# Performance work log

Measured on AMD Instinct MI355X. Metric: run time of the kernel, lower is better.

The kernel has to match this reference:

```python
import jax, jax.numpy as jnp
import numpy as np

B, L, C = 2, 2048, 1024
H = 16
D = C // H  # 64
MAX_SCALE_MUL = float(np.log(100.0))
EPS = 1e-12


def setup_inputs() -> dict:
    key = jax.random.key(0)
    ks = jax.random.split(key, 6)
    x = jax.random.normal(ks[0], (B, L, C), dtype=jnp.float32)
    attn_bias = jax.random.normal(ks[1], (1, 1, L, L), dtype=jnp.float32) * 0.02
    W_qkv = jax.random.normal(ks[2], (3 * C, C), dtype=jnp.float32) * (1.0 / np.sqrt(C))
    q_bias = jnp.zeros((C,), dtype=jnp.float32)
    v_bias = jnp.zeros((C,), dtype=jnp.float32)
    scale_mul = jnp.full((1, H, 1, 1), np.log(4.0), dtype=jnp.float32)
    W_proj = jax.random.normal(ks[3], (C, C), dtype=jnp.float32) * (1.0 / np.sqrt(C))
    b_proj = jnp.zeros((C,), dtype=jnp.float32)
    return {"x": x, "attn_bias": attn_bias, "W_qkv": W_qkv, "q_bias": q_bias,
            "v_bias": v_bias, "scale_mul": scale_mul, "W_proj": W_proj, "b_proj": b_proj}


def _l2norm(t):
    # F.normalize(dim=-1): x / max(||x||_2, eps)
    n = jnp.sqrt(jnp.sum(t * t, axis=-1, keepdims=True))
    return t / jnp.maximum(n, EPS)


def reference(x, attn_bias, W_qkv, q_bias, v_bias, scale_mul, W_proj, b_proj):
    bias = jnp.concatenate([q_bias, jnp.zeros_like(q_bias), v_bias])  # (3C,)
    qkv = x @ W_qkv.T + bias                     # (B, L, 3C)
    qkv = qkv.reshape(B, L, 3, H, D)
    q, k, v = jnp.moveaxis(qkv, 2, 0)            # each (B, L, H, D)
    q = jnp.transpose(q, (0, 2, 1, 3))           # (B, H, L, D)
    k = jnp.transpose(k, (0, 2, 1, 3))
    v = jnp.transpose(v, (0, 2, 1, 3))
    # attn_l2_norm path: scale = 1, learned per-head scale clamped at log(100)
    sm = jnp.exp(jnp.minimum(scale_mul, MAX_SCALE_MUL))  # (1, H, 1, 1)
    q = _l2norm(q) * sm
    k = _l2norm(k)
    scores = jnp.einsum('bhqd,bhkd->bhqk', q, k) + attn_bias  # scale=1
    attn = jax.nn.softmax(scores, axis=-1)
    out = jnp.einsum('bhqk,bhkd->bhqd', attn, v)  # (B, H, L, D)
    out = jnp.transpose(out, (0, 2, 1, 3)).reshape(B, L, C)
    return out @ W_proj.T + b_proj
```

## Files before the change

kernel.cpp:

```cpp
#include <hip/hip_runtime.h>


typedef __bf16 bf16x8 __attribute__((ext_vector_type(8)));
typedef __bf16 bf16x4 __attribute__((ext_vector_type(4)));
typedef float  f32x4  __attribute__((ext_vector_type(4)));

#define BB 2
#define LL 2048
#define CC 1024
#define HH 16
#define DD 64
#define LOG2E 1.44269504088896f

__device__ __forceinline__ f32x4 mfma_16x16x32(bf16x8 a, bf16x8 b, f32x4 c) {
    return __builtin_amdgcn_mfma_f32_16x16x32_bf16(a, b, c, 0, 0, 0);
}

__device__ __forceinline__ void gload_lds16(const __bf16* g, __bf16* lds) {
    __builtin_amdgcn_global_load_lds(
        (const __attribute__((address_space(1))) unsigned int*)g,
        (__attribute__((address_space(3))) unsigned int*)lds,
        16, 0, 0);
}

__device__ __forceinline__ unsigned pk_bf16(float a, float b) {
    unsigned short ua = __builtin_bit_cast(unsigned short, (__bf16)a);
    unsigned short ub = __builtin_bit_cast(unsigned short, (__bf16)b);
    return (unsigned)ua | ((unsigned)ub << 16);
}

__global__ __launch_bounds__(256) void cvt3_kernel(
    const float* __restrict__ x, const float* __restrict__ wq, const float* __restrict__ wp,
    __bf16* __restrict__ xb, __bf16* __restrict__ wqb, __bf16* __restrict__ wpb) {
    const int i = blockIdx.x * 256 + threadIdx.x;
    const float* src; __bf16* dst; int off;
    if (i < 1048576)      { src = x;  dst = xb;  off = i; }
    else if (i < 1835008) { src = wq; dst = wqb; off = i - 1048576; }
    else                  { src = wp; dst = wpb; off = i - 1835008; }
    float4 v = reinterpret_cast<const float4*>(src)[off];
    bf16x4 o;
    o[0] = (__bf16)v.x; o[1] = (__bf16)v.y; o[2] = (__bf16)v.z; o[3] = (__bf16)v.w;
    reinterpret_cast<bf16x4*>(dst)[off] = o;
}

__global__ __launch_bounds__(256) void gemm_qkv_fused_kernel(
    const __bf16* __restrict__ A, const __bf16* __restrict__ Bm,
    const float* __restrict__ q_bias, const float* __restrict__ v_bias,
    const float* __restrict__ scale_mul,
    __bf16* __restrict__ Qw, __bf16* __restrict__ Kw, __bf16* __restrict__ Vw) {
    __shared__ __bf16 As[128 * 64];
    __shared__ __bf16 Bs[128 * 64];
    const int tid = threadIdx.x;
    const int K = 1024;
    const int nwg = gridDim.x * gridDim.y;
    const int flat = blockIdx.y * gridDim.x + blockIdx.x;
    const int wg = (flat & 7) * (nwg >> 3) + (flat >> 3);
    const int m0 = (wg % gridDim.x) * 128, n0 = (wg / gridDim.x) * 128;
    const int w  = tid >> 6, l = tid & 63;
    const int wr = (w >> 1) * 64, wc = (w & 1) * 64;
    const int lr = l & 15, lg = l >> 4;
    const int rmask = (lr & 7) << 4;
    f32x4 acc[4][4] = {};
    const int lrow = l >> 3;
    const int celem = (((l & 7) ^ lrow) << 3);

    for (int kt = 0; kt < K; kt += 64) {
        __syncthreads();
#pragma unroll
        for (int i = 0; i < 4; ++i) {
            const int row = w * 32 + i * 8;
            gload_lds16(A + (size_t)(m0 + row + lrow) * K + kt + celem, &As[row * 64]);
            gload_lds16(Bm + (size_t)(n0 + row + lrow) * K + kt + celem, &Bs[row * 64]);
        }
        asm volatile("s_waitcnt vmcnt(0)" ::: "memory");
        __syncthreads();
#pragma unroll
        for (int kk = 0; kk < 2; ++kk) {
            bf16x8 af[4], bfr[4];
#pragma unroll
            for (int m = 0; m < 4; ++m)
                af[m] = *reinterpret_cast<const bf16x8*>(
                    (char*)As + (wr + m * 16 + lr) * 128 + ((kk * 64 + lg * 16) ^ rmask));
#pragma unroll
            for (int n = 0; n < 4; ++n)
                bfr[n] = *reinterpret_cast<const bf16x8*>(
                    (char*)Bs + (wc + n * 16 + lr) * 128 + ((kk * 64 + lg * 16) ^ rmask));
#pragma unroll
            for (int m = 0; m < 4; ++m)
#pragma unroll
                for (int n = 0; n < 4; ++n)
                    acc[m][n] = mfma_16x16x32(af[m], bfr[n], acc[m][n]);
        }
    }

    const int gcbase = n0 + wc;
    const int type = gcbase >> 10;
    const int h = (gcbase & 1023) >> 6;
    float qscale = 1.0f;
    if (type == 0) qscale = __expf(fminf(scale_mul[h], 4.60517019f)) * LOG2E;
    __bf16* dst = (type == 0) ? Qw : (type == 1) ? Kw : Vw;

#pragma unroll
    for (int m = 0; m < 4; ++m) {
        if (type != 1) {
            const float* bptr = (type == 0) ? q_bias : v_bias;
#pragma unroll
            for (int n = 0; n < 4; ++n) {
                float bv = bptr[(gcbase & 1023) + n * 16 + lr];
#pragma unroll
                for (int r = 0; r < 4; ++r) acc[m][n][r] += bv;
            }
        }
        float rs[4];
        if (type < 2) {
#pragma unroll
            for (int r = 0; r < 4; ++r) {
                float ss = 0.f;
#pragma unroll
                for (int n = 0; n < 4; ++n) ss += acc[m][n][r] * acc[m][n][r];
                rs[r] = ss;
            }
#pragma unroll
            for (int off = 1; off < 16; off <<= 1)
#pragma unroll
                for (int r = 0; r < 4; ++r) rs[r] += __shfl_xor(rs[r], off, 64);
#pragma unroll
            for (int r = 0; r < 4; ++r)
                rs[r] = ((type == 0) ? qscale : 1.0f) / fmaxf(sqrtf(rs[r]), 1e-12f);
        } else {
#pragma unroll
            for (int r = 0; r < 4; ++r) rs[r] = 1.0f;
        }
        const int rowg = m0 + wr + m * 16 + lg * 4;
#pragma unroll
        for (int n = 0; n < 4; ++n) {
            const int d = n * 16 + lr;
#pragma unroll
            for (int r = 0; r < 4; ++r) {
                const int row = rowg + r;
                const int bb = row >> 11, ll = row & 2047;
                dst[((size_t)((bb << 4) + h) * 2048 + ll) * 64 + d] =
                    (__bf16)(acc[m][n][r] * rs[r]);
            }
        }
    }
}

__global__ __launch_bounds__(256) void gemm_proj_kernel(
    const __bf16* __restrict__ A, const __bf16* __restrict__ Bm,
    float* __restrict__ Cf, const float* __restrict__ bias, int M, int N, int K) {
    __shared__ __bf16 As[128 * 64];
    __shared__ __bf16 Bs[128 * 64];
    const int tid = threadIdx.x;
    const int nwg = gridDim.x * gridDim.y;
    const int flat = blockIdx.y * gridDim.x + blockIdx.x;
    const int wg = (flat & 7) * (nwg >> 3) + (flat >> 3);
    const int m0 = (wg % gridDim.x) * 128, n0 = (wg / gridDim.x) * 128;
    const int w  = tid >> 6, l = tid & 63;
    const int wr = (w >> 1) * 64, wc = (w & 1) * 64;
    const int lr = l & 15, lg = l >> 4;
    const int rmask = (lr & 7) << 4;
    f32x4 acc[4][4] = {};
    const int lrow = l >> 3;
    const int celem = (((l & 7) ^ lrow) << 3);

    for (int kt = 0; kt < K; kt += 64) {
        __syncthreads();
#pragma unroll
        for (int i = 0; i < 4; ++i) {
            const int row = w * 32 + i * 8;
            gload_lds16(A + (size_t)(m0 + row + lrow) * K + kt + celem, &As[row * 64]);
            gload_lds16(Bm + (size_t)(n0 + row + lrow) * K + kt + celem, &Bs[row * 64]);
        }
        asm volatile("s_waitcnt vmcnt(0)" ::: "memory");
        __syncthreads();
#pragma unroll
        for (int kk = 0; kk < 2; ++kk) {
            bf16x8 af[4], bfr[4];
#pragma unroll
            for (int m = 0; m < 4; ++m)
                af[m] = *reinterpret_cast<const bf16x8*>(
                    (char*)As + (wr + m * 16 + lr) * 128 + ((kk * 64 + lg * 16) ^ rmask));
#pragma unroll
            for (int n = 0; n < 4; ++n)
                bfr[n] = *reinterpret_cast<const bf16x8*>(
                    (char*)Bs + (wc + n * 16 + lr) * 128 + ((kk * 64 + lg * 16) ^ rmask));
#pragma unroll
            for (int m = 0; m < 4; ++m)
#pragma unroll
                for (int n = 0; n < 4; ++n)
                    acc[m][n] = mfma_16x16x32(af[m], bfr[n], acc[m][n]);
        }
    }
#pragma unroll
    for (int m = 0; m < 4; ++m)
#pragma unroll
        for (int n = 0; n < 4; ++n) {
            const int row = m0 + wr + m * 16 + lg * 4;
            const int col = n0 + wc + n * 16 + lr;
#pragma unroll
            for (int r = 0; r < 4; ++r)
                Cf[(size_t)(row + r) * N + col] = acc[m][n][r] + bias[col];
        }
}

__global__ __launch_bounds__(256) void prep_kernel(
    const float* __restrict__ bias, __bf16* __restrict__ bias_bf,
    const __bf16* __restrict__ Vin, __bf16* __restrict__ Vp) {
    const int tid = threadIdx.x;
    if (blockIdx.x < 2048) {
        __shared__ float wmax[4];
        const int l = blockIdx.x;
        const int w = tid >> 6;
        float4 a = reinterpret_cast<const float4*>(bias + (size_t)l * 2048)[tid];
        float4 b = reinterpret_cast<const float4*>(bias + (size_t)l * 2048 + 1024)[tid];
        float m = fmaxf(fmaxf(fmaxf(a.x, a.y), fmaxf(a.z, a.w)),
                        fmaxf(fmaxf(b.x, b.y), fmaxf(b.z, b.w)));
#pragma unroll
        for (int off = 1; off < 64; off <<= 1) m = fmaxf(m, __shfl_xor(m, off, 64));
        if ((tid & 63) == 0) wmax[w] = m;
        __syncthreads();
        float M = fmaxf(fmaxf(wmax[0], wmax[1]), fmaxf(wmax[2], wmax[3]));
        bf16x4 o0, o1;
        o0[0] = (__bf16)((a.x - M) * LOG2E); o0[1] = (__bf16)((a.y - M) * LOG2E);
        o0[2] = (__bf16)((a.z - M) * LOG2E); o0[3] = (__bf16)((a.w - M) * LOG2E);
        o1[0] = (__bf16)((b.x - M) * LOG2E); o1[1] = (__bf16)((b.y - M) * LOG2E);
        o1[2] = (__bf16)((b.z - M) * LOG2E); o1[3] = (__bf16)((b.w - M) * LOG2E);
        reinterpret_cast<bf16x4*>(bias_bf + (size_t)l * 2048)[tid] = o0;
        reinterpret_cast<bf16x4*>(bias_bf + (size_t)l * 2048 + 1024)[tid] = o1;
    } else {
        __shared__ __bf16 T[64][72];
        const int idx = blockIdx.x - 2048;
        const int lb = idx & 31, bh = idx >> 5;
        const size_t base = (size_t)bh * LL * DD;
        const int row = tid >> 2, c = (tid & 3) * 16;
        {
            const __bf16* src = Vin + base + (size_t)(lb * 64 + row) * 64 + c;
            *reinterpret_cast<bf16x8*>(&T[row][c])     = *reinterpret_cast<const bf16x8*>(src);
            *reinterpret_cast<bf16x8*>(&T[row][c + 8]) = *reinterpret_cast<const bf16x8*>(src + 8);
        }
        __syncthreads();
        __bf16 val[16];
#pragma unroll
        for (int jj = 0; jj < 16; ++jj) {
            const int cp = c + jj;
            const int wb = cp & 31;
            const int kloc = (cp & ~31) | (((wb >> 3) & 3) << 2) | (((wb >> 2) & 1) << 4) | (wb & 3);
            val[jj] = T[kloc][row];
        }
        __bf16* dst = Vp + base + (size_t)row * 2048 + lb * 64 + c;
        *reinterpret_cast<bf16x8*>(dst)     = *reinterpret_cast<bf16x8*>(&val[0]);
        *reinterpret_cast<bf16x8*>(dst + 8) = *reinterpret_cast<bf16x8*>(&val[8]);
    }
}

__global__ __launch_bounds__(512, 6) void attn_kernel(
    const __bf16* __restrict__ Q, const __bf16* __restrict__ K,
    const __bf16* __restrict__ Vp, const __bf16* __restrict__ biasB,
    float* __restrict__ Of0, float* __restrict__ Of1, float* __restrict__ lsF) {
    __shared__ __bf16 KVs[2][2][64 * 64];
    const int bh = blockIdx.x, qb = blockIdx.y, sp = blockIdx.z;
    const int tid = threadIdx.x;
    const int w = tid >> 6, l = tid & 63;
    const int lr = l & 15, lg = l >> 4;
    const int rmask = (lr & 7) << 4;
    const int b = bh >> 4, h = bh & 15;
    const size_t base = (size_t)bh * LL * DD;
    const int kb0 = sp * 16;

    const int gq = qb * 128 + w * 16 + lr;
    bf16x8 qf[2];
    qf[0] = *reinterpret_cast<const bf16x8*>(Q + base + (size_t)gq * 64 + lg * 8);
    qf[1] = *reinterpret_cast<const bf16x8*>(Q + base + (size_t)gq * 64 + 32 + lg * 8);
    const __bf16* brow = biasB + (size_t)gq * 2048 + lg * 4;

    bf16x8 ones;
#pragma unroll
    for (int j = 0; j < 8; ++j) ones[j] = (__bf16)1.0f;

    const int srow = w * 8 + (l >> 3);
    const int sce  = (l & 7) * 8;
    const int smask = (srow & 7) << 4;
    const __bf16* kgbase = K  + base + (size_t)srow * 64   + sce;
    const __bf16* vgbase = Vp + base + (size_t)srow * 2048 + sce;

    bf16x8 k0, v0;
    auto stage_regs = [&](int kb) {
        k0 = *reinterpret_cast<const bf16x8*>(kgbase + (size_t)kb * 64 * 64);
        v0 = *reinterpret_cast<const bf16x8*>(vgbase + kb * 64);
    };
    auto write_lds = [&](int buf) {
        *reinterpret_cast<bf16x8*>((char*)KVs[buf][0] + srow * 128 + ((sce * 2) ^ smask)) = k0;
        *reinterpret_cast<bf16x8*>((char*)KVs[buf][1] + srow * 128 + ((sce * 2) ^ smask)) = v0;
    };

    stage_regs(kb0);
    write_lds(0);

    f32x4 Oa[4] = {};
    f32x4 ls = {};
    int cur = 0;

    bf16x4 bcur[4];
#pragma unroll
    for (int t = 0; t < 4; ++t)
        bcur[t] = *reinterpret_cast<const bf16x4*>(brow + kb0 * 64 + t * 16);

    for (int kb = 0; kb < 16; ++kb) {
        __syncthreads();
        if (kb < 15) stage_regs(kb0 + kb + 1);

        bf16x4 bnext[4];
        if (kb < 15) {
#pragma unroll
            for (int t = 0; t < 4; ++t)
                bnext[t] = *reinterpret_cast<const bf16x4*>(brow + (kb0 + kb + 1) * 64 + t * 16);
        }

        const char* Kc = (const char*)KVs[cur][0];
        const char* Vc = (const char*)KVs[cur][1];

        f32x4 sa[4];
#pragma unroll
        for (int t = 0; t < 4; ++t)
#pragma unroll
            for (int r = 0; r < 4; ++r)
                sa[t][r] = (float)bcur[t][r];

#pragma unroll
        for (int t = 0; t < 4; ++t) {
            const char* kr = Kc + (t * 16 + lr) * 128;
            bf16x8 kf0 = *reinterpret_cast<const bf16x8*>(kr + ((lg * 16) ^ rmask));
            bf16x8 kf1 = *reinterpret_cast<const bf16x8*>(kr + ((64 + lg * 16) ^ rmask));
            sa[t] = mfma_16x16x32(kf0, qf[0], sa[t]);
            sa[t] = mfma_16x16x32(kf1, qf[1], sa[t]);
        }

        float p[4][4];
#pragma unroll
        for (int t = 0; t < 4; ++t)
#pragma unroll
            for (int r = 0; r < 4; ++r)
                p[t][r] = exp2f(sa[t][r]);
        union Upa { unsigned u[4]; bf16x8 v; } pa0, pa1;
        pa0.u[0] = pk_bf16(p[0][0], p[0][1]); pa0.u[1] = pk_bf16(p[0][2], p[0][3]);
        pa0.u[2] = pk_bf16(p[1][0], p[1][1]); pa0.u[3] = pk_bf16(p[1][2], p[1][3]);
        pa1.u[0] = pk_bf16(p[2][0], p[2][1]); pa1.u[1] = pk_bf16(p[2][2], p[2][3]);
        pa1.u[2] = pk_bf16(p[3][0], p[3][1]); pa1.u[3] = pk_bf16(p[3][2], p[3][3]);

        ls = mfma_16x16x32(pa0.v, ones, ls);
        ls = mfma_16x16x32(pa1.v, ones, ls);

#pragma unroll
        for (int t = 0; t < 4; ++t) {
            const char* vr = Vc + (t * 16 + lr) * 128;
            bf16x8 vf0 = *reinterpret_cast<const bf16x8*>(vr + ((lg * 16) ^ rmask));
            bf16x8 vf1 = *reinterpret_cast<const bf16x8*>(vr + ((64 + lg * 16) ^ rmask));
            Oa[t] = mfma_16x16x32(pa0.v, vf0, Oa[t]);
            Oa[t] = mfma_16x16x32(pa1.v, vf1, Oa[t]);
        }

        if (kb < 15) {
            write_lds(cur ^ 1);
#pragma unroll
            for (int t = 0; t < 4; ++t) bcur[t] = bnext[t];
        }
        cur ^= 1;
    }

    float* Ofp = sp ? Of1 : Of0;
#pragma unroll
    for (int t = 0; t < 4; ++t)
#pragma unroll
        for (int r = 0; r < 4; ++r) {
            const int row = qb * 128 + w * 16 + lg * 4 + r;
            Ofp[((size_t)(b * 2048 + row)) * 1024 + h * 64 + t * 16 + lr] = Oa[t][r];
        }
    if (lr == 0) {
#pragma unroll
        for (int r = 0; r < 4; ++r) {
            const int row = qb * 128 + w * 16 + lg * 4 + r;
            lsF[((size_t)sp * 32 + bh) * 2048 + row] = ls[r];
        }
    }
}

__global__ __launch_bounds__(256) void combine_kernel(
    const float* __restrict__ Of0, const float* __restrict__ Of1,
    const float* __restrict__ lsF, __bf16* __restrict__ Oc) {
    const int i = blockIdx.x * 256 + threadIdx.x;
    const int e = i * 4;
    const int row = e >> 10;
    const int col = e & 1023;
    const int h = col >> 6;
    const int b = row >> 11, l = row & 2047;
    const size_t lsi = ((size_t)(b * 16 + h)) * 2048 + l;
    const float inv = 1.0f / (lsF[lsi] + lsF[(size_t)32 * 2048 + lsi]);
    float4 a = reinterpret_cast<const float4*>(Of0)[i];
    float4 c = reinterpret_cast<const float4*>(Of1)[i];
    bf16x4 o;
    o[0] = (__bf16)((a.x + c.x) * inv);
    o[1] = (__bf16)((a.y + c.y) * inv);
    o[2] = (__bf16)((a.z + c.z) * inv);
    o[3] = (__bf16)((a.w + c.w) * inv);
    reinterpret_cast<bf16x4*>(Oc)[i] = o;
}

extern "C" void kernel_launch(void* const* d_in, const int* in_sizes, int n_in,
                              void* d_out, int out_size, void* d_ws, size_t ws_size,
                              hipStream_t stream) {
    const float* x         = (const float*)d_in[0];
    const float* attn_bias = (const float*)d_in[1];
    const float* W_qkv     = (const float*)d_in[2];
    const float* q_bias    = (const float*)d_in[3];
    const float* v_bias    = (const float*)d_in[4];
    const float* scale_mul = (const float*)d_in[5];
    const float* W_proj    = (const float*)d_in[6];
    const float* b_proj    = (const float*)d_in[7];
    float* out = (float*)d_out;

    char* ws = (char*)d_ws;
    size_t off = 0;
    auto alloc = [&](size_t bytes) {
        void* p = ws + off;
        off = (off + bytes + 255) & ~(size_t)255;
        return p;
    };
    __bf16* Vw      = (__bf16*)alloc((size_t)BB * HH * LL * DD * 2);
    __bf16* xb      = (__bf16*)alloc((size_t)4096 * 1024 * 2);
    __bf16* wqkvb   = (__bf16*)alloc((size_t)3072 * 1024 * 2);
    __bf16* wprojb  = (__bf16*)alloc((size_t)1024 * 1024 * 2);
    __bf16* Qw      = (__bf16*)alloc((size_t)BB * HH * LL * DD * 2);
    __bf16* Kw      = (__bf16*)alloc((size_t)BB * HH * LL * DD * 2);
    __bf16* Oc      = (__bf16*)alloc((size_t)4096 * 1024 * 2);
    __bf16* biasB   = (__bf16*)alloc((size_t)2048 * 2048 * 2);
    __bf16* Vp      = (__bf16*)alloc((size_t)BB * HH * LL * DD * 2);
    float*  Of1     = (float*)alloc((size_t)4096 * 1024 * 4);
    float*  lsF     = (float*)alloc((size_t)2 * 32 * 2048 * 4);
    float*  Of0     = (float*)d_ws;

    cvt3_kernel<<<8192, 256, 0, stream>>>(x, W_qkv, W_proj, xb, wqkvb, wprojb);

    gemm_qkv_fused_kernel<<<dim3(32, 24), 256, 0, stream>>>(
        xb, wqkvb, q_bias, v_bias, scale_mul, Qw, Kw, Vw);

    prep_kernel<<<3072, 256, 0, stream>>>(attn_bias, biasB, Vw, Vp);

    attn_kernel<<<dim3(32, 16, 2), 512, 0, stream>>>(Qw, Kw, Vp, biasB, Of0, Of1, lsF);

    combine_kernel<<<4096, 256, 0, stream>>>(Of0, Of1, lsF, Oc);

    gemm_proj_kernel<<<dim3(32, 8), 256, 0, stream>>>(
        Oc, wprojb, out, b_proj, 4096, 1024, 1024);
}
```

Measured before the change: 179.6 us.

## Drop split-K attention and fuse normalization into attention epilogue

Result: faster. 167.5 us (-6.7%).

```diff
diff --git a/kernel.cpp b/kernel.cpp
--- a/kernel.cpp
+++ b/kernel.cpp
@@ -257,16 +257,15 @@
 __global__ __launch_bounds__(512, 6) void attn_kernel(
     const __bf16* __restrict__ Q, const __bf16* __restrict__ K,
     const __bf16* __restrict__ Vp, const __bf16* __restrict__ biasB,
-    float* __restrict__ Of0, float* __restrict__ Of1, float* __restrict__ lsF) {
+    __bf16* __restrict__ Octx) {
     __shared__ __bf16 KVs[2][2][64 * 64];
-    const int bh = blockIdx.x, qb = blockIdx.y, sp = blockIdx.z;
+    const int bh = blockIdx.x, qb = blockIdx.y;
     const int tid = threadIdx.x;
     const int w = tid >> 6, l = tid & 63;
     const int lr = l & 15, lg = l >> 4;
     const int rmask = (lr & 7) << 4;
     const int b = bh >> 4, h = bh & 15;
     const size_t base = (size_t)bh * LL * DD;
-    const int kb0 = sp * 16;
 
     const int gq = qb * 128 + w * 16 + lr;
     bf16x8 qf[2];
@@ -294,7 +293,7 @@
         *reinterpret_cast<bf16x8*>((char*)KVs[buf][1] + srow * 128 + ((sce * 2) ^ smask)) = v0;
     };
 
-    stage_regs(kb0);
+    stage_regs(0);
     write_lds(0);
 
     f32x4 Oa[4] = {};
@@ -304,17 +303,17 @@
     bf16x4 bcur[4];
 #pragma unroll
     for (int t = 0; t < 4; ++t)
-        bcur[t] = *reinterpret_cast<const bf16x4*>(brow + kb0 * 64 + t * 16);
-
-    for (int kb = 0; kb < 16; ++kb) {
-        __syncthreads();
-        if (kb < 15) stage_regs(kb0 + kb + 1);
+        bcur[t] = *reinterpret_cast<const bf16x4*>(brow + t * 16);
+
+    for (int kb = 0; kb < 32; ++kb) {
+        __syncthreads();
+        if (kb < 31) stage_regs(kb + 1);
 
         bf16x4 bnext[4];
-        if (kb < 15) {
+        if (kb < 31) {
 #pragma unroll
             for (int t = 0; t < 4; ++t)
-                bnext[t] = *reinterpret_cast<const bf16x4*>(brow + (kb0 + kb + 1) * 64 + t * 16);
+                bnext[t] = *reinterpret_cast<const bf16x4*>(brow + (kb + 1) * 64 + t * 16);
         }
 
         const char* Kc = (const char*)KVs[cur][0];
@@ -360,7 +359,7 @@
             Oa[t] = mfma_16x16x32(pa1.v, vf1, Oa[t]);
         }
 
-        if (kb < 15) {
+        if (kb < 31) {
             write_lds(cur ^ 1);
 #pragma unroll
             for (int t = 0; t < 4; ++t) bcur[t] = bnext[t];
@@ -368,42 +367,17 @@
         cur ^= 1;
     }
 
-    float* Ofp = sp ? Of1 : Of0;
+    float inv[4];
+#pragma unroll
+    for (int r = 0; r < 4; ++r) inv[r] = 1.0f / ls[r];
 #pragma unroll
     for (int t = 0; t < 4; ++t)
 #pragma unroll
         for (int r = 0; r < 4; ++r) {
             const int row = qb * 128 + w * 16 + lg * 4 + r;
-            Ofp[((size_t)(b * 2048 + row)) * 1024 + h * 64 + t * 16 + lr] = Oa[t][r];
-        }
-    if (lr == 0) {
-#pragma unroll
-        for (int r = 0; r < 4; ++r) {
-            const int row = qb * 128 + w * 16 + lg * 4 + r;
-            lsF[((size_t)sp * 32 + bh) * 2048 + row] = ls[r];
-        }
-    }
-}
-
-__global__ __launch_bounds__(256) void combine_kernel(
-    const float* __restrict__ Of0, const float* __restrict__ Of1,
-    const float* __restrict__ lsF, __bf16* __restrict__ Oc) {
-    const int i = blockIdx.x * 256 + threadIdx.x;
-    const int e = i * 4;
-    const int row = e >> 10;
-    const int col = e & 1023;
-    const int h = col >> 6;
-    const int b = row >> 11, l = row & 2047;
-    const size_t lsi = ((size_t)(b * 16 + h)) * 2048 + l;
-    const float inv = 1.0f / (lsF[lsi] + lsF[(size_t)32 * 2048 + lsi]);
-    float4 a = reinterpret_cast<const float4*>(Of0)[i];
-    float4 c = reinterpret_cast<const float4*>(Of1)[i];
-    bf16x4 o;
-    o[0] = (__bf16)((a.x + c.x) * inv);
-    o[1] = (__bf16)((a.y + c.y) * inv);
-    o[2] = (__bf16)((a.z + c.z) * inv);
-    o[3] = (__bf16)((a.w + c.w) * inv);
-    reinterpret_cast<bf16x4*>(Oc)[i] = o;
+            Octx[((size_t)(b * 2048 + row)) * 1024 + h * 64 + t * 16 + lr] =
+                (__bf16)(Oa[t][r] * inv[r]);
+        }
 }
 
 extern "C" void kernel_launch(void* const* d_in, const int* in_sizes, int n_in,
@@ -435,9 +409,6 @@
     __bf16* Oc      = (__bf16*)alloc((size_t)4096 * 1024 * 2);
     __bf16* biasB   = (__bf16*)alloc((size_t)2048 * 2048 * 2);
     __bf16* Vp      = (__bf16*)alloc((size_t)BB * HH * LL * DD * 2);
-    float*  Of1     = (float*)alloc((size_t)4096 * 1024 * 4);
-    float*  lsF     = (float*)alloc((size_t)2 * 32 * 2048 * 4);
-    float*  Of0     = (float*)d_ws;
 
     cvt3_kernel<<<8192, 256, 0, stream>>>(x, W_qkv, W_proj, xb, wqkvb, wprojb);
 
@@ -446,9 +417,7 @@
 
     prep_kernel<<<3072, 256, 0, stream>>>(attn_bias, biasB, Vw, Vp);
 
-    attn_kernel<<<dim3(32, 16, 2), 512, 0, stream>>>(Qw, Kw, Vp, biasB, Of0, Of1, lsF);
-
-    combine_kernel<<<4096, 256, 0, stream>>>(Of0, Of1, lsF, Oc);
+    attn_kernel<<<dim3(32, 16), 512, 0, stream>>>(Qw, Kw, Vp, biasB, Oc);
 
     gemm_proj_kernel<<<dim3(32, 8), 256, 0, stream>>>(
         Oc, wprojb, out, b_proj, 4096, 1024, 1024);
```
